# Kernel optimization log

Hardware: AMD Instinct MI355X
Metric: run time of the kernel (lower is better)

The kernel has to match this reference:

```python
import jax, jax.numpy as jnp
import numpy as np

N_NODES = 50000
N_EDGES = 800000
D_IN = 256
D_HID = 256
N_CLASSES = 10
N_GRAPHS = 512
LN_EPS = 1e-5


def gcn_conv(x, edge_index, W, b, num_nodes):
    # PyG GCNConv (default settings): h = x @ W; add self-loops; symmetric
    # deg^{-1/2} normalization; sum-aggregate messages; add bias.
    h = x @ W                                   # [N, H]
    loop = jnp.arange(num_nodes, dtype=edge_index.dtype)
    src = jnp.concatenate([edge_index[0], loop])  # [E+N]
    dst = jnp.concatenate([edge_index[1], loop])  # [E+N]
    deg = jax.ops.segment_sum(jnp.ones_like(dst, dtype=h.dtype), dst,
                              num_segments=num_nodes)
    dinv = jnp.where(deg > 0, jax.lax.rsqrt(deg), 0.0)
    norm = dinv[src] * dinv[dst]                # [E+N]
    msg = h[src] * norm[:, None]                # gather + scale
    out = jax.ops.segment_sum(msg, dst, num_segments=num_nodes)  # scatter-add
    return out + b


def layer_norm(x, w, b):
    mu = jnp.mean(x, axis=-1, keepdims=True)
    var = jnp.mean(jnp.square(x - mu), axis=-1, keepdims=True)
    return (x - mu) * jax.lax.rsqrt(var + LN_EPS) * w + b


def global_mean_pool(x, batch, num_graphs):
    s = jax.ops.segment_sum(x, batch, num_segments=num_graphs)
    cnt = jax.ops.segment_sum(jnp.ones_like(batch, dtype=x.dtype), batch,
                              num_segments=num_graphs)
    return s / jnp.maximum(cnt, 1.0)[:, None]


def setup_inputs() -> dict:
    key = jax.random.key(0)
    ks = jax.random.split(key, 12)
    x = jax.random.normal(ks[0], (N_NODES, D_IN), dtype=jnp.float32)
    edge_index = jax.random.randint(ks[1], (2, N_EDGES), 0, N_NODES, dtype=jnp.int32)
    batch = jnp.sort(jax.random.randint(ks[2], (N_NODES,), 0, N_GRAPHS, dtype=jnp.int32))
    s_in = 1.0 / np.sqrt(D_IN)
    s_hid = 1.0 / np.sqrt(D_HID)
    return {
        "x": x,
        "edge_index": edge_index,
        "batch": batch,
        "W1": jax.random.uniform(ks[3], (D_IN, D_HID), jnp.float32, -s_in, s_in),
        "b1": jnp.zeros((D_HID,), jnp.float32),
        "W2": jax.random.uniform(ks[4], (D_HID, D_HID), jnp.float32, -s_hid, s_hid),
        "b2": jnp.zeros((D_HID,), jnp.float32),
        "ln1_w": jnp.ones((D_HID,), jnp.float32),
        "ln1_b": jnp.zeros((D_HID,), jnp.float32),
        "ln2_w": jnp.ones((D_HID,), jnp.float32),
        "ln2_b": jnp.zeros((D_HID,), jnp.float32),
        "lin_W": jax.random.uniform(ks[5], (D_HID, N_CLASSES), jnp.float32, -s_hid, s_hid),
        "lin_b": jnp.zeros((N_CLASSES,), jnp.float32),
    }


def reference(x, edge_index, batch, W1, b1, W2, b2, ln1_w, ln1_b, ln2_w, ln2_b, lin_W, lin_b):
    # dropout is identity at inference (training=False)
    h = gcn_conv(x, edge_index, W1, b1, N_NODES)
    h = jax.nn.relu(layer_norm(h, ln1_w, ln1_b))
    h = gcn_conv(h, edge_index, W2, b2, N_NODES)
    h = jax.nn.relu(layer_norm(h, ln2_w, ln2_b))
    pooled = global_mean_pool(h, batch, N_GRAPHS)   # [G, H]
    return pooled @ lin_W + lin_b                   # [G, C]
```

## Files before the change

kernel.cpp:

```cpp
#include <hip/hip_runtime.h>
#include <hip/hip_fp8.h>
#include <stdint.h>

#define D 256
#define CAP 64

typedef __attribute__((ext_vector_type(8))) short short8;
typedef __attribute__((ext_vector_type(4))) float f32x4;

#define SW(n, c) (((n) << 8) + ((((c) ^ ((n) & 15))) << 3))

__device__ inline unsigned short f2bf(float f) {
    uint32_t u = __builtin_bit_cast(uint32_t, f);
    uint32_t r = (u + 0x7FFFu + ((u >> 16) & 1u)) >> 16;
    return (unsigned short)r;
}

__device__ inline float bf2f(unsigned short b) {
    return __builtin_bit_cast(float, (uint32_t)b << 16);
}

__device__ inline f32x4 fp8x4_to_f32(uint32_t v) {
    __hip_fp8x4_e4m3 a;
    a.__x = v;
    float4 f = (float4)a;
    return (f32x4){f.x, f.y, f.z, f.w};
}

__device__ inline uint8_t f32_to_fp8(float f) {
    __hip_fp8_e4m3 q(f);
    return (uint8_t)q.__x;
}

__global__ __launch_bounds__(256) void k_prep(const float* __restrict__ x,
                                              unsigned short* __restrict__ xb, int n8,
                                              const float* __restrict__ W1,
                                              const float* __restrict__ W2,
                                              unsigned short* __restrict__ Wt1,
                                              unsigned short* __restrict__ Wt2,
                                              int* __restrict__ cur,
                                              int nNodes, int nf2b) {
    int b = blockIdx.x, t = threadIdx.x;
    if (b < nf2b) {
        int i = b * 256 + t;
        if (i < n8) {
            f32x4 v0 = ((const f32x4*)x)[i * 2];
            f32x4 v1 = ((const f32x4*)x)[i * 2 + 1];
            short8 o;
            o[0] = (short)f2bf(v0.x); o[1] = (short)f2bf(v0.y);
            o[2] = (short)f2bf(v0.z); o[3] = (short)f2bf(v0.w);
            o[4] = (short)f2bf(v1.x); o[5] = (short)f2bf(v1.y);
            o[6] = (short)f2bf(v1.z); o[7] = (short)f2bf(v1.w);
            ((short8*)xb)[i] = o;
        }
    } else if (b < nf2b + 512) {
        int idx = (b - nf2b) * 256 + t;
        int w = idx >> 16;
        int r = idx & 65535;
        int n = r >> 8, k = r & 255;
        const float* W = w ? W2 : W1;
        unsigned short* Wt = w ? Wt2 : Wt1;
        Wt[n * 256 + k] = f2bf(W[k * 256 + n]);
    } else {
        int i = (b - nf2b - 512) * 256 + t;
        if (i < nNodes) cur[i] = 0;
    }
}

__global__ __launch_bounds__(256) void k_dinv(const int* __restrict__ cur,
                                              float* __restrict__ dinv, int n) {
    int i = blockIdx.x * 256 + threadIdx.x;
    if (i < n) dinv[i] = rsqrtf((float)(cur[i] + 1));
}


__device__ __forceinline__ void gemm_body(unsigned short* sm, int gid,
                                          const unsigned short* __restrict__ A,
                                          const unsigned short* __restrict__ Bt,
                                          uint8_t* __restrict__ Cb, int M) {
    int t = threadIdx.x;
    int wave = t >> 6, lane = t & 63;
    int quad = lane >> 4, l16 = lane & 15;
    int mr = wave >> 1, nc = wave & 1;
    int bm = (gid >> 1) * 128;
    int bn = (gid & 1) * 128;

    {
        int c = t & 31;
        int r0 = t >> 5;
#pragma unroll
        for (int j = 0; j < 16; ++j) {
            int r = r0 + j * 8;
            uint4 v = *reinterpret_cast<const uint4*>(Bt + (size_t)(bn + r) * D + c * 8);
            *reinterpret_cast<uint4*>(sm + SW(r, c)) = v;
        }
    }

    uint4 af[4][8];
#pragma unroll
    for (int tm = 0; tm < 4; ++tm) {
        int row = bm + mr * 64 + tm * 16 + l16;
        if (row >= M) row = M - 1;
        const unsigned short* ap = A + (size_t)row * D + quad * 8;
#pragma unroll
        for (int ks = 0; ks < 8; ++ks)
            af[tm][ks] = *reinterpret_cast<const uint4*>(ap + ks * 32);
    }
    __syncthreads();

    f32x4 acc[4][4];
#pragma unroll
    for (int tm = 0; tm < 4; ++tm)
#pragma unroll
        for (int tn = 0; tn < 4; ++tn) acc[tm][tn] = (f32x4){0.f, 0.f, 0.f, 0.f};

#pragma unroll
    for (int ks = 0; ks < 8; ++ks) {
        short8 b[4];
#pragma unroll
        for (int tn = 0; tn < 4; ++tn) {
            int n = nc * 64 + tn * 16 + l16;
            b[tn] = *reinterpret_cast<const short8*>(sm + SW(n, ks * 4 + quad));
        }
#pragma unroll
        for (int tm = 0; tm < 4; ++tm) {
            short8 a = __builtin_bit_cast(short8, af[tm][ks]);
#pragma unroll
            for (int tn = 0; tn < 4; ++tn)
                acc[tm][tn] = __builtin_amdgcn_mfma_f32_16x16x32_bf16(a, b[tn], acc[tm][tn], 0, 0, 0);
        }
    }
    __syncthreads();

    uint8_t (*sC)[136] = reinterpret_cast<uint8_t (*)[136]>(sm);
#pragma unroll
    for (int tm = 0; tm < 4; ++tm) {
        int rb = mr * 64 + tm * 16 + quad * 4;
#pragma unroll
        for (int tn = 0; tn < 4; ++tn) {
            int cc = nc * 64 + tn * 16 + l16;
#pragma unroll
            for (int r = 0; r < 4; ++r)
                sC[rb + r][cc] = f32_to_fp8(acc[tm][tn][r]);
        }
    }
    __syncthreads();

#pragma unroll
    for (int it = 0; it < 4; ++it) {
        int idx = it * 256 + t;
        int r = idx >> 3, ch = idx & 7;
        int gr = bm + r;
        if (gr < M)
            *reinterpret_cast<uint4*>(Cb + (size_t)gr * D + bn + ch * 16) =
                *reinterpret_cast<const uint4*>(&sC[r][ch * 16]);
    }
}

__device__ __forceinline__ void fill_body(int fid,
                                          const int* __restrict__ src,
                                          const int* __restrict__ dst,
                                          int* __restrict__ cur,
                                          int* __restrict__ ewi, int ne) {
    int i = (fid * 256 + threadIdx.x) * 4;
    if (i + 4 <= ne) {
        int4 s4 = *reinterpret_cast<const int4*>(src + i);
        int4 d4 = *reinterpret_cast<const int4*>(dst + i);
        int p;
        p = atomicAdd(&cur[d4.x], 1);
        if (p < CAP) ewi[d4.x * CAP + p] = s4.x;
        p = atomicAdd(&cur[d4.y], 1);
        if (p < CAP) ewi[d4.y * CAP + p] = s4.y;
        p = atomicAdd(&cur[d4.z], 1);
        if (p < CAP) ewi[d4.z * CAP + p] = s4.z;
        p = atomicAdd(&cur[d4.w], 1);
        if (p < CAP) ewi[d4.w * CAP + p] = s4.w;
    } else {
        for (int j = i; j < ne; ++j) {
            int s = src[j], d = dst[j];
            int p = atomicAdd(&cur[d], 1);
            if (p < CAP) ewi[d * CAP + p] = s;
        }
    }
}

__global__ __launch_bounds__(256, 2) void k_gemmfill(const unsigned short* __restrict__ A,
                                                     const unsigned short* __restrict__ Bt,
                                                     uint8_t* __restrict__ Cb, int M,
                                                     const int* __restrict__ src,
                                                     const int* __restrict__ dst,
                                                     int* __restrict__ cur,
                                                     int* __restrict__ ewi, int ne,
                                                     int NI, int ngemm) {
    __shared__ unsigned short sm[32768];
    int b = blockIdx.x;
    if (b < 2 * NI) {
        if (b & 1) fill_body(b >> 1, src, dst, cur, ewi, ne);
        else       gemm_body(sm, b >> 1, A, Bt, Cb, M);
    } else {
        int r = b - 2 * NI;
        if (ngemm > NI) gemm_body(sm, NI + r, A, Bt, Cb, M);
        else            fill_body(NI + r, src, dst, cur, ewi, ne);
    }
}

__global__ __launch_bounds__(256, 2) void k_gemm(const unsigned short* __restrict__ A,
                                                 const unsigned short* __restrict__ Bt,
                                                 uint8_t* __restrict__ Cb, int M) {
    __shared__ unsigned short sm[32768];
    gemm_body(sm, blockIdx.x, A, Bt, Cb, M);
}

__global__ __launch_bounds__(256) void k_agg(const uint8_t* __restrict__ hb,
                                             const int* __restrict__ cur,
                                             const float* __restrict__ dinv,
                                             const int* __restrict__ ewi,
                                             const float* __restrict__ bias,
                                             const float* __restrict__ lnw,
                                             const float* __restrict__ lnb,
                                             unsigned short* __restrict__ out, int n) {
    __shared__ int2 lew[4][CAP];
    int wave = threadIdx.x >> 6, lane = threadIdx.x & 63;
    int node = blockIdx.x * 4 + wave;
    if (node >= n) return;
    int cnt = min(cur[node], CAP);
    if (lane < cnt) {
        int s = ewi[node * CAP + lane];
        int2 p;
        p.x = s * 64;
        p.y = __builtin_bit_cast(int, dinv[s]);
        lew[wave][lane] = p;
    }
    __builtin_amdgcn_wave_barrier();

    float di = dinv[node];
    const uint32_t* hb32 = (const uint32_t*)hb;
    uint32_t rs = hb32[(uint32_t)node * 64 + lane];
    f32x4 acc = (f32x4){0.f, 0.f, 0.f, 0.f};
    const int2* lep = lew[wave];
    int nq = cnt >> 2;

    int2 p0, p1, p2, p3;
    if (nq > 0) { p0 = lep[0]; p1 = lep[1]; p2 = lep[2]; p3 = lep[3]; }
    int q = 0;
#pragma unroll 1
    for (; q + 1 < nq; ++q) {
        int b4 = (q + 1) * 4;
        uint32_t r0 = hb32[(uint32_t)(p0.x + lane)];
        uint32_t r1 = hb32[(uint32_t)(p1.x + lane)];
        uint32_t r2 = hb32[(uint32_t)(p2.x + lane)];
        uint32_t r3 = hb32[(uint32_t)(p3.x + lane)];
        int2 n0 = lep[b4], n1 = lep[b4 + 1], n2 = lep[b4 + 2], n3 = lep[b4 + 3];
        acc += fp8x4_to_f32(r0) * __builtin_bit_cast(float, p0.y);
        acc += fp8x4_to_f32(r1) * __builtin_bit_cast(float, p1.y);
        acc += fp8x4_to_f32(r2) * __builtin_bit_cast(float, p2.y);
        acc += fp8x4_to_f32(r3) * __builtin_bit_cast(float, p3.y);
        p0 = n0; p1 = n1; p2 = n2; p3 = n3;
    }
    if (nq > 0) {
        uint32_t r0 = hb32[(uint32_t)(p0.x + lane)];
        uint32_t r1 = hb32[(uint32_t)(p1.x + lane)];
        uint32_t r2 = hb32[(uint32_t)(p2.x + lane)];
        uint32_t r3 = hb32[(uint32_t)(p3.x + lane)];
        acc += fp8x4_to_f32(r0) * __builtin_bit_cast(float, p0.y);
        acc += fp8x4_to_f32(r1) * __builtin_bit_cast(float, p1.y);
        acc += fp8x4_to_f32(r2) * __builtin_bit_cast(float, p2.y);
        acc += fp8x4_to_f32(r3) * __builtin_bit_cast(float, p3.y);
    }
    for (int e = nq * 4; e < cnt; ++e) {
        int2 p = lep[e];
        uint32_t r = hb32[(uint32_t)(p.x + lane)];
        acc += fp8x4_to_f32(r) * __builtin_bit_cast(float, p.y);
    }

    f32x4 self = fp8x4_to_f32(rs);
    f32x4 b4v = ((const f32x4*)bias)[lane];
    f32x4 v = self * (di * di) + acc * di + b4v;

    float s1 = v.x + v.y + v.z + v.w;
    float s2 = v.x * v.x + v.y * v.y + v.z * v.z + v.w * v.w;
#pragma unroll
    for (int o = 32; o > 0; o >>= 1) {
        s1 += __shfl_xor(s1, o, 64);
        s2 += __shfl_xor(s2, o, 64);
    }
    float mean = s1 * (1.0f / 256.0f);
    float var = s2 * (1.0f / 256.0f) - mean * mean;
    float inv = rsqrtf(var + 1e-5f);
    f32x4 w4 = ((const f32x4*)lnw)[lane];
    f32x4 lb = ((const f32x4*)lnb)[lane];
    float y0 = fmaxf((v.x - mean) * inv * w4.x + lb.x, 0.f);
    float y1 = fmaxf((v.y - mean) * inv * w4.y + lb.y, 0.f);
    float y2 = fmaxf((v.z - mean) * inv * w4.z + lb.z, 0.f);
    float y3 = fmaxf((v.w - mean) * inv * w4.w + lb.w, 0.f);
    uint2 w;
    w.x = (uint32_t)f2bf(y0) | ((uint32_t)f2bf(y1) << 16);
    w.y = (uint32_t)f2bf(y2) | ((uint32_t)f2bf(y3) << 16);
    *reinterpret_cast<uint2*>(out + (size_t)node * D + lane * 4) = w;
}

__global__ __launch_bounds__(256) void k_pool(const unsigned short* __restrict__ h,
                                              const int* __restrict__ batch,
                                              const float* __restrict__ linW,
                                              const float* __restrict__ linb,
                                              float* __restrict__ out,
                                              int nNodes) {
    int g = blockIdx.x, t = threadIdx.x;
    int lo = 0, hi = nNodes;
    while (lo < hi) { int m = (lo + hi) >> 1; if (batch[m] < g) lo = m + 1; else hi = m; }
    int lo2 = lo, hi2 = nNodes;
    while (lo2 < hi2) { int m = (lo2 + hi2) >> 1; if (batch[m] < g + 1) lo2 = m + 1; else hi2 = m; }
    float s0 = 0.f, s1 = 0.f, s2 = 0.f, s3 = 0.f;
    int i = lo;
    for (; i + 4 <= lo2; i += 4) {
        s0 += bf2f(h[(size_t)(i + 0) * D + t]);
        s1 += bf2f(h[(size_t)(i + 1) * D + t]);
        s2 += bf2f(h[(size_t)(i + 2) * D + t]);
        s3 += bf2f(h[(size_t)(i + 3) * D + t]);
    }
    for (; i < lo2; ++i) s0 += bf2f(h[(size_t)i * D + t]);
    float s = (s0 + s1) + (s2 + s3);
    float cnt = (float)(lo2 - lo);
    float pooled = s / fmaxf(cnt, 1.f);
    __shared__ float sp[256];
    __shared__ float red[4];
    sp[t] = pooled;
    __syncthreads();
    for (int c = 0; c < 10; ++c) {
        float v = sp[t] * linW[t * 10 + c];
#pragma unroll
        for (int o = 32; o > 0; o >>= 1) v += __shfl_xor(v, o, 64);
        if ((t & 63) == 0) red[t >> 6] = v;
        __syncthreads();
        if (t == 0) out[g * 10 + c] = red[0] + red[1] + red[2] + red[3] + linb[c];
        __syncthreads();
    }
}

extern "C" void kernel_launch(void* const* d_in, const int* in_sizes, int n_in,
                              void* d_out, int out_size, void* d_ws, size_t ws_size,
                              hipStream_t stream) {
    const float* x    = (const float*)d_in[0];
    const int*   ei   = (const int*)d_in[1];
    const int*   batch= (const int*)d_in[2];
    const float* W1   = (const float*)d_in[3];
    const float* b1   = (const float*)d_in[4];
    const float* W2   = (const float*)d_in[5];
    const float* b2   = (const float*)d_in[6];
    const float* ln1w = (const float*)d_in[7];
    const float* ln1b = (const float*)d_in[8];
    const float* ln2w = (const float*)d_in[9];
    const float* ln2b = (const float*)d_in[10];
    const float* linW = (const float*)d_in[11];
    const float* linb = (const float*)d_in[12];
    float* out = (float*)d_out;

    int nNodes  = in_sizes[0] / D;
    int nEdges  = in_sizes[1] / 2;
    int nGraphs = out_size / 10;

    const int* src = ei;
    const int* dst = ei + nEdges;

    char* ws = (char*)d_ws;
    size_t o = 0;
    auto alloc = [&](size_t bytes) -> char* {
        char* p = ws + o;
        o += (bytes + 511) & ~(size_t)511;
        return p;
    };
    unsigned short* xb = (unsigned short*)alloc((size_t)nNodes * D * 2);
    uint8_t* hW = (uint8_t*)alloc((size_t)nNodes * D);
    unsigned short* h1 = (unsigned short*)alloc((size_t)nNodes * D * 2);
    int* cur   = (int*)alloc((size_t)nNodes * 4);
    float* dinv= (float*)alloc((size_t)nNodes * 4);
    int* ewi   = (int*)alloc((size_t)nNodes * CAP * 4);
    unsigned short* Wt1 = (unsigned short*)alloc((size_t)D * D * 2);
    unsigned short* Wt2 = (unsigned short*)alloc((size_t)D * D * 2);
    (void)ws_size;

    int gn = (nNodes + 255) / 256;
    int ge4 = (nEdges / 4 + 255) / 256;
    int n8 = nNodes * (D / 8);
    int nf2b = (n8 + 255) / 256;
    int ngemm = ((nNodes + 127) / 128) * 2;
    int NI = min(ngemm, ge4);

    k_prep<<<nf2b + 512 + gn, 256, 0, stream>>>(x, xb, n8, W1, W2, Wt1, Wt2,
                                                cur, nNodes, nf2b);
    k_gemmfill<<<ngemm + ge4, 256, 0, stream>>>(xb, Wt1, hW, nNodes,
                                                src, dst, cur, ewi, nEdges,
                                                NI, ngemm);
    k_dinv<<<gn, 256, 0, stream>>>(cur, dinv, nNodes);

    k_agg<<<(nNodes + 3) / 4, 256, 0, stream>>>(hW, cur, dinv, ewi,
                                                b1, ln1w, ln1b, h1, nNodes);
    k_gemm<<<ngemm, 256, 0, stream>>>(h1, Wt2, hW, nNodes);
    k_agg<<<(nNodes + 3) / 4, 256, 0, stream>>>(hW, cur, dinv, ewi,
                                                b2, ln2w, ln2b, xb, nNodes);
    k_pool<<<nGraphs, 256, 0, stream>>>(xb, batch, linW, linb, out, nNodes);
}
```

Before: 273.7 us.

## Halve GEMM LDS footprint via two-pass K staging and fold dinv into aggregation

The GEMM body now stages the B tile in two K-halves of 128 columns using a smaller swizzle, which halves shared memory per block (64KB to 32KB). This may let more blocks fit per CU at the cost of an extra barrier pair. Separately, the k_dinv kernel and its buffer are removed. k_agg now computes rsqrt(deg+1) inline from cur, which saves a launch and an array write but recomputes it per edge in both aggregation passes.

```diff
diff --git a/kernel.cpp b/kernel.cpp
--- a/kernel.cpp
+++ b/kernel.cpp
@@ -8,7 +8,7 @@
 typedef __attribute__((ext_vector_type(8))) short short8;
 typedef __attribute__((ext_vector_type(4))) float f32x4;
 
-#define SW(n, c) (((n) << 8) + ((((c) ^ ((n) & 15))) << 3))
+#define SW2(n, c) (((n) << 7) + ((((c) ^ ((n) & 7))) << 3))
 
 __device__ inline unsigned short f2bf(float f) {
     uint32_t u = __builtin_bit_cast(uint32_t, f);
@@ -67,12 +67,6 @@
     }
 }
 
-__global__ __launch_bounds__(256) void k_dinv(const int* __restrict__ cur,
-                                              float* __restrict__ dinv, int n) {
-    int i = blockIdx.x * 256 + threadIdx.x;
-    if (i < n) dinv[i] = rsqrtf((float)(cur[i] + 1));
-}
-
 
 __device__ __forceinline__ void gemm_body(unsigned short* sm, int gid,
                                           const unsigned short* __restrict__ A,
@@ -85,17 +79,6 @@
     int bm = (gid >> 1) * 128;
     int bn = (gid & 1) * 128;
 
-    {
-        int c = t & 31;
-        int r0 = t >> 5;
-#pragma unroll
-        for (int j = 0; j < 16; ++j) {
-            int r = r0 + j * 8;
-            uint4 v = *reinterpret_cast<const uint4*>(Bt + (size_t)(bn + r) * D + c * 8);
-            *reinterpret_cast<uint4*>(sm + SW(r, c)) = v;
-        }
-    }
-
     uint4 af[4][8];
 #pragma unroll
     for (int tm = 0; tm < 4; ++tm) {
@@ -106,7 +89,6 @@
         for (int ks = 0; ks < 8; ++ks)
             af[tm][ks] = *reinterpret_cast<const uint4*>(ap + ks * 32);
     }
-    __syncthreads();
 
     f32x4 acc[4][4];
 #pragma unroll
@@ -115,22 +97,38 @@
         for (int tn = 0; tn < 4; ++tn) acc[tm][tn] = (f32x4){0.f, 0.f, 0.f, 0.f};
 
 #pragma unroll
-    for (int ks = 0; ks < 8; ++ks) {
-        short8 b[4];
-#pragma unroll
-        for (int tn = 0; tn < 4; ++tn) {
-            int n = nc * 64 + tn * 16 + l16;
-            b[tn] = *reinterpret_cast<const short8*>(sm + SW(n, ks * 4 + quad));
-        }
-#pragma unroll
-        for (int tm = 0; tm < 4; ++tm) {
-            short8 a = __builtin_bit_cast(short8, af[tm][ks]);
-#pragma unroll
-            for (int tn = 0; tn < 4; ++tn)
-                acc[tm][tn] = __builtin_amdgcn_mfma_f32_16x16x32_bf16(a, b[tn], acc[tm][tn], 0, 0, 0);
-        }
-    }
-    __syncthreads();
+    for (int half = 0; half < 2; ++half) {
+        {
+            int c = t & 15;
+            int r0 = t >> 4;
+#pragma unroll
+            for (int j = 0; j < 8; ++j) {
+                int r = r0 + j * 16;
+                uint4 v = *reinterpret_cast<const uint4*>(
+                    Bt + (size_t)(bn + r) * D + half * 128 + c * 8);
+                *reinterpret_cast<uint4*>(sm + SW2(r, c)) = v;
+            }
+        }
+        __syncthreads();
+#pragma unroll
+        for (int ks = 0; ks < 4; ++ks) {
+            int gks = half * 4 + ks;
+            short8 b[4];
+#pragma unroll
+            for (int tn = 0; tn < 4; ++tn) {
+                int n = nc * 64 + tn * 16 + l16;
+                b[tn] = *reinterpret_cast<const short8*>(sm + SW2(n, ks * 4 + quad));
+            }
+#pragma unroll
+            for (int tm = 0; tm < 4; ++tm) {
+                short8 a = __builtin_bit_cast(short8, af[tm][gks]);
+#pragma unroll
+                for (int tn = 0; tn < 4; ++tn)
+                    acc[tm][tn] = __builtin_amdgcn_mfma_f32_16x16x32_bf16(a, b[tn], acc[tm][tn], 0, 0, 0);
+            }
+        }
+        __syncthreads();
+    }
 
     uint8_t (*sC)[136] = reinterpret_cast<uint8_t (*)[136]>(sm);
 #pragma unroll
@@ -192,7 +190,7 @@
                                                      int* __restrict__ cur,
                                                      int* __restrict__ ewi, int ne,
                                                      int NI, int ngemm) {
-    __shared__ unsigned short sm[32768];
+    __shared__ unsigned short sm[16384];
     int b = blockIdx.x;
     if (b < 2 * NI) {
         if (b & 1) fill_body(b >> 1, src, dst, cur, ewi, ne);
@@ -207,13 +205,12 @@
 __global__ __launch_bounds__(256, 2) void k_gemm(const unsigned short* __restrict__ A,
                                                  const unsigned short* __restrict__ Bt,
                                                  uint8_t* __restrict__ Cb, int M) {
-    __shared__ unsigned short sm[32768];
+    __shared__ unsigned short sm[16384];
     gemm_body(sm, blockIdx.x, A, Bt, Cb, M);
 }
 
 __global__ __launch_bounds__(256) void k_agg(const uint8_t* __restrict__ hb,
                                              const int* __restrict__ cur,
-                                             const float* __restrict__ dinv,
                                              const int* __restrict__ ewi,
                                              const float* __restrict__ bias,
                                              const float* __restrict__ lnw,
@@ -223,17 +220,18 @@
     int wave = threadIdx.x >> 6, lane = threadIdx.x & 63;
     int node = blockIdx.x * 4 + wave;
     if (node >= n) return;
-    int cnt = min(cur[node], CAP);
+    int cdeg = cur[node];
+    int cnt = min(cdeg, CAP);
     if (lane < cnt) {
         int s = ewi[node * CAP + lane];
         int2 p;
         p.x = s * 64;
-        p.y = __builtin_bit_cast(int, dinv[s]);
+        p.y = __builtin_bit_cast(int, rsqrtf((float)(cur[s] + 1)));
         lew[wave][lane] = p;
     }
     __builtin_amdgcn_wave_barrier();
 
-    float di = dinv[node];
+    float di = rsqrtf((float)(cdeg + 1));
     const uint32_t* hb32 = (const uint32_t*)hb;
     uint32_t rs = hb32[(uint32_t)node * 64 + lane];
     f32x4 acc = (f32x4){0.f, 0.f, 0.f, 0.f};
@@ -373,7 +371,6 @@
     uint8_t* hW = (uint8_t*)alloc((size_t)nNodes * D);
     unsigned short* h1 = (unsigned short*)alloc((size_t)nNodes * D * 2);
     int* cur   = (int*)alloc((size_t)nNodes * 4);
-    float* dinv= (float*)alloc((size_t)nNodes * 4);
     int* ewi   = (int*)alloc((size_t)nNodes * CAP * 4);
     unsigned short* Wt1 = (unsigned short*)alloc((size_t)D * D * 2);
     unsigned short* Wt2 = (unsigned short*)alloc((size_t)D * D * 2);
@@ -391,12 +388,10 @@
     k_gemmfill<<<ngemm + ge4, 256, 0, stream>>>(xb, Wt1, hW, nNodes,
                                                 src, dst, cur, ewi, nEdges,
                                                 NI, ngemm);
-    k_dinv<<<gn, 256, 0, stream>>>(cur, dinv, nNodes);
-
-    k_agg<<<(nNodes + 3) / 4, 256, 0, stream>>>(hW, cur, dinv, ewi,
+    k_agg<<<(nNodes + 3) / 4, 256, 0, stream>>>(hW, cur, ewi,
                                                 b1, ln1w, ln1b, h1, nNodes);
     k_gemm<<<ngemm, 256, 0, stream>>>(h1, Wt2, hW, nNodes);
-    k_agg<<<(nNodes + 3) / 4, 256, 0, stream>>>(hW, cur, dinv, ewi,
+    k_agg<<<(nNodes + 3) / 4, 256, 0, stream>>>(hW, cur, ewi,
                                                 b2, ln2w, ln2b, xb, nNodes);
     k_pool<<<nGraphs, 256, 0, stream>>>(xb, batch, linW, linb, out, nNodes);
 }
```

Result: no change. 269.6 us (-1.5%).
